# Performance work log

Measured on AMD Instinct MI355X. Metric: run time of the kernel, lower is better.

## Reference

```python
import jax, jax.numpy as jnp
import numpy as np

B, D, T = 16, 512, 2048
H = 2
HD = D // H

def setup_inputs() -> dict:
    key = jax.random.key(0)
    k1, k2, k3, k4 = jax.random.split(key, 4)
    s_in = 1.0 / np.sqrt(D)   # torch default-like uniform init for weight_matrix
    s_t = 1.0 / np.sqrt(T)    # nn.Linear default init bound
    xs = jax.random.normal(k1, (B, D, T), dtype=jnp.float32)
    W_KQ = jax.random.uniform(k2, (D, D), jnp.float32, -s_in, s_in)
    W_PV = jax.random.uniform(k3, (D, D), jnp.float32, -s_in, s_in)
    W_out = jax.random.uniform(k4, (T, T), jnp.float32, -s_t, s_t)
    return {"xs": xs, "W_KQ": W_KQ, "W_PV": W_PV, "W_out": W_out}

def reference(xs, W_KQ, W_PV, W_out):
    b, d, t = xs.shape
    xs_skip = xs[:, :, :-1]                                   # [B, D, T-1]
    # xskq = xs_skip^T @ W_KQ  -> [B, T-1, D]
    xskq = jnp.einsum('bds,dj->bsj', xs_skip, W_KQ)
    # split heads: [B, H, T-1, HD]
    xskq_split = xskq.reshape(b, t - 1, H, HD).transpose(0, 2, 1, 3)
    # xs reshaped to heads along feature dim: [B, H, HD, T]
    xs_r = xs.reshape(b, H, HD, t)
    attn_arg = jnp.matmul(xskq_split, xs_r)                   # [B, H, T-1, T], rho=1
    # NON-STANDARD: softmax over the head axis (size 2)
    sm = jax.nn.softmax(attn_arg, axis=1)
    # W_PV @ xs_skip -> [B, D, T-1], split into heads [B, H, HD, T-1]
    wpvx = jnp.einsum('id,bds->bis', W_PV, xs_skip).reshape(b, H, HD, t - 1)
    f_attn = jnp.matmul(wpvx, sm).reshape(b, d, t)            # [B, D, T]
    # output = Linear(T, T, bias=None) then take last token:
    # out[b, i] = sum_t f_attn[b, i, t] * W_out[T-1, t]
    out = jnp.einsum('bdt,t->bd', f_attn, W_out[-1])
    return out
```

## Files before the change

kernel.cpp:

```cpp
#include <hip/hip_runtime.h>
#include <hip/hip_bf16.h>

#define NB 16
#define ND 512
#define NT 2048
#define TM1 2047
#define NHD 256

typedef __attribute__((ext_vector_type(8))) short bf16x8;
typedef __attribute__((ext_vector_type(4))) float f32x4;
typedef unsigned short ushort_t;
typedef unsigned int uint_t;

#define G0_OFF    0ull
#define G0_ELEMS  (16ull * 2047ull)
#define R0_OFF    32768ull
#define SX_OFF    40960ull
#define ZERO_FLOATS 49152ull
#define WSUM_OFF  49152ull
#define WKQT_OFF  49408ull
#define CHUNK_OFF 180480ull
#define BATCH_US  (2048ull * 512ull)
#define BATCH_FLOATS (2ull * 524288ull)

__device__ __forceinline__ ushort_t f2bf(float x) {
    union { float f; uint_t u; } v; v.f = x;
    uint_t r = v.u + 0x7FFFu + ((v.u >> 16) & 1u);
    return (ushort_t)(r >> 16);
}
__device__ __forceinline__ float bf2f(uint_t u) {
    union { uint_t u; float f; } v; v.u = u << 16;
    return v.f;
}

__device__ __forceinline__ void async_copy16(const ushort_t* g, ushort_t* l) {
    __builtin_amdgcn_global_load_lds(
        (const __attribute__((address_space(1))) void*)g,
        (__attribute__((address_space(3))) void*)l, 16, 0, 0);
}

__global__ __launch_bounds__(256) void k_prep(const float* __restrict__ wkq,
                                              ushort_t* __restrict__ wkqT,
                                              const float* __restrict__ wlast,
                                              float* __restrict__ wsum,
                                              float* __restrict__ zbase) {
    __shared__ float tile[32][33];
    const int j0 = blockIdx.x * 32, d0 = blockIdx.y * 32;
    const int c = threadIdx.x & 31, r = threadIdx.x >> 5;
    #pragma unroll
    for (int i = 0; i < 4; ++i) {
        const int d = r + i * 8;
        tile[d][c] = wkq[(size_t)(d0 + d) * ND + j0 + c];
    }
    __syncthreads();
    #pragma unroll
    for (int i = 0; i < 4; ++i) {
        const int j = r + i * 8;
        wkqT[(size_t)(j0 + j) * ND + d0 + c] = f2bf(tile[c][j]);
    }
    const int bid = blockIdx.y * 16 + blockIdx.x;
    if (threadIdx.x < 192) zbase[bid * 192 + threadIdx.x] = 0.f;
    if (bid == 0) {
        __shared__ float red[256];
        float s = 0.f;
        for (int t = threadIdx.x; t < NT; t += 256) s += wlast[t];
        red[threadIdx.x] = s;
        __syncthreads();
        for (int off = 128; off > 0; off >>= 1) {
            if (threadIdx.x < off) red[threadIdx.x] += red[threadIdx.x + off];
            __syncthreads();
        }
        if (threadIdx.x == 0) *wsum = red[0];
    }
}

__global__ __launch_bounds__(256) void k_cvt_xst(const float* __restrict__ xs,
                                                 ushort_t* __restrict__ xst, int b0) {
    __shared__ float tile[64][257];
    const int t0 = blockIdx.x * 256, d0 = blockIdx.y * 64;
    const int cc = blockIdx.z;
    const float* xb = xs + (size_t)(b0 + cc) * ND * NT;
    ushort_t* xo = xst + (size_t)cc * BATCH_US;
    const int wave = threadIdx.x >> 6, lane = threadIdx.x & 63;
    #pragma unroll
    for (int i = 0; i < 16; ++i) {
        const int row = wave * 16 + i;
        *(float4*)&tile[row][lane * 4] =
            *(const float4*)&xb[(size_t)(d0 + row) * NT + t0 + lane * 4];
    }
    __syncthreads();
    const int c8 = (threadIdx.x & 7) * 8;
    #pragma unroll
    for (int i = 0; i < 8; ++i) {
        const int t = i * 32 + (threadIdx.x >> 3);
        uint_t w[4];
        #pragma unroll
        for (int p = 0; p < 4; ++p)
            w[p] = (uint_t)f2bf(tile[c8 + 2 * p][t]) |
                   ((uint_t)f2bf(tile[c8 + 2 * p + 1][t]) << 16);
        *(uint4*)&xo[(size_t)(t0 + t) * ND + d0 + c8] = *(uint4*)w;
    }
}

__global__ __launch_bounds__(256) void k_qd(const ushort_t* __restrict__ xst,
                                            const ushort_t* __restrict__ wkqT,
                                            ushort_t* __restrict__ qdb) {
    const int j0 = blockIdx.x * 128;
    const int s0 = blockIdx.y * 128;
    const int cc = blockIdx.z;
    __shared__ __align__(16) ushort_t As[128 * 64];
    __shared__ __align__(16) ushort_t Bs[128 * 64];
    const int tid = threadIdx.x;
    const int wave = tid >> 6, lane = tid & 63;
    const int l15 = lane & 15, quad = lane >> 4;
    const int wm = wave >> 1, wn = wave & 1;
    const int swz = l15 & 7;
    const int lrow = lane >> 3;
    const size_t lsrc = (size_t)lrow * ND + (size_t)(((lane & 7) ^ lrow) << 3);
    const ushort_t* xa = xst + (size_t)cc * BATCH_US + (size_t)s0 * ND;
    const ushort_t* wb = wkqT + (size_t)j0 * ND;
    ushort_t* qo = qdb + (size_t)cc * BATCH_US;
    f32x4 acc[4][4];
    #pragma unroll
    for (int mi = 0; mi < 4; ++mi)
        #pragma unroll
        for (int nj = 0; nj < 4; ++nj) acc[mi][nj] = (f32x4){0.f, 0.f, 0.f, 0.f};
    for (int ks = 0; ks < 8; ++ks) {
        const int k0 = ks * 64;
        #pragma unroll
        for (int n = 0; n < 4; ++n) {
            const int rbase = wave * 32 + n * 8;
            async_copy16(xa + (size_t)rbase * ND + k0 + lsrc, &As[rbase * 64]);
            async_copy16(wb + (size_t)rbase * ND + k0 + lsrc, &Bs[rbase * 64]);
        }
        __builtin_amdgcn_s_waitcnt(0);
        __syncthreads();
        #pragma unroll
        for (int kc = 0; kc < 2; ++kc) {
            bf16x8 af[4], bfr[4];
            #pragma unroll
            for (int mi = 0; mi < 4; ++mi)
                af[mi] = *(const bf16x8*)&As[(wm * 64 + mi * 16 + l15) * 64 + (((kc * 4 + quad) ^ swz) << 3)];
            #pragma unroll
            for (int nj = 0; nj < 4; ++nj)
                bfr[nj] = *(const bf16x8*)&Bs[(wn * 64 + nj * 16 + l15) * 64 + (((kc * 4 + quad) ^ swz) << 3)];
            #pragma unroll
            for (int mi = 0; mi < 4; ++mi)
                #pragma unroll
                for (int nj = 0; nj < 4; ++nj)
                    acc[mi][nj] = __builtin_amdgcn_mfma_f32_16x16x32_bf16(af[mi], bfr[nj], acc[mi][nj], 0, 0, 0);
        }
        __syncthreads();
    }
    #pragma unroll
    for (int mi = 0; mi < 4; ++mi) {
        const int srow = s0 + wm * 64 + mi * 16 + quad * 4;
        #pragma unroll
        for (int nj = 0; nj < 4; ++nj) {
            const int jcol = j0 + wn * 64 + nj * 16 + l15;
            const float sgn = (jcol < NHD) ? 1.f : -1.f;
            #pragma unroll
            for (int r = 0; r < 4; ++r)
                qo[(size_t)(srow + r) * ND + jcol] = f2bf(sgn * acc[mi][nj][r]);
        }
    }
}

__global__ __launch_bounds__(256) void k_attn(const ushort_t* __restrict__ qdb,
                                              const ushort_t* __restrict__ xst,
                                              const float* __restrict__ wlast,
                                              float* __restrict__ g0, int b0) {
    const int t0 = blockIdx.x * 128;
    const int s0 = blockIdx.y * 128;
    const int cc = blockIdx.z;
    const int b = b0 + cc;
    __shared__ __align__(16) ushort_t As[128 * 64];
    __shared__ __align__(16) ushort_t Bs[128 * 64];
    const int tid = threadIdx.x;
    const int wave = tid >> 6, lane = tid & 63;
    const int l15 = lane & 15, quad = lane >> 4;
    const int wm = wave >> 1, wn = wave & 1;
    const int swz = l15 & 7;
    const int lrow = lane >> 3;
    const size_t lsrc = (size_t)lrow * ND + (size_t)(((lane & 7) ^ lrow) << 3);
    const ushort_t* qa = qdb + (size_t)cc * BATCH_US + (size_t)s0 * ND;
    const ushort_t* xa = xst + (size_t)cc * BATCH_US + (size_t)t0 * ND;
    f32x4 acc[4][4];
    #pragma unroll
    for (int mi = 0; mi < 4; ++mi)
        #pragma unroll
        for (int nj = 0; nj < 4; ++nj) acc[mi][nj] = (f32x4){0.f, 0.f, 0.f, 0.f};
    for (int ks = 0; ks < 8; ++ks) {
        const int k0 = ks * 64;
        #pragma unroll
        for (int n = 0; n < 4; ++n) {
            const int rbase = wave * 32 + n * 8;
            async_copy16(qa + (size_t)rbase * ND + k0 + lsrc, &As[rbase * 64]);
            async_copy16(xa + (size_t)rbase * ND + k0 + lsrc, &Bs[rbase * 64]);
        }
        __builtin_amdgcn_s_waitcnt(0);
        __syncthreads();
        #pragma unroll
        for (int kc = 0; kc < 2; ++kc) {
            bf16x8 af[4], bfr[4];
            #pragma unroll
            for (int mi = 0; mi < 4; ++mi)
                af[mi] = *(const bf16x8*)&As[(wm * 64 + mi * 16 + l15) * 64 + (((kc * 4 + quad) ^ swz) << 3)];
            #pragma unroll
            for (int nj = 0; nj < 4; ++nj)
                bfr[nj] = *(const bf16x8*)&Bs[(wn * 64 + nj * 16 + l15) * 64 + (((kc * 4 + quad) ^ swz) << 3)];
            #pragma unroll
            for (int mi = 0; mi < 4; ++mi)
                #pragma unroll
                for (int nj = 0; nj < 4; ++nj)
                    acc[mi][nj] = __builtin_amdgcn_mfma_f32_16x16x32_bf16(af[mi], bfr[nj], acc[mi][nj], 0, 0, 0);
        }
        __syncthreads();
    }
    float gp[4][4] = {};
    #pragma unroll
    for (int nj = 0; nj < 4; ++nj) {
        const float wt = wlast[t0 + wn * 64 + nj * 16 + l15];
        #pragma unroll
        for (int mi = 0; mi < 4; ++mi)
            #pragma unroll
            for (int r = 0; r < 4; ++r) {
                const float e = __expf(-acc[mi][nj][r]);
                const float sg = __builtin_amdgcn_rcpf(1.f + e);
                gp[mi][r] = fmaf(sg, wt, gp[mi][r]);
            }
    }
    #pragma unroll
    for (int mi = 0; mi < 4; ++mi)
        #pragma unroll
        for (int r = 0; r < 4; ++r) {
            float v = gp[mi][r];
            v += __shfl_xor(v, 1);
            v += __shfl_xor(v, 2);
            v += __shfl_xor(v, 4);
            v += __shfl_xor(v, 8);
            if (l15 == 0) {
                const int srow = s0 + wm * 64 + mi * 16 + quad * 4 + r;
                if (srow < TM1) atomicAdd(&g0[b * TM1 + srow], v);
            }
        }
}

__global__ __launch_bounds__(256) void k_r(const ushort_t* __restrict__ xst,
                                           const float* __restrict__ g0,
                                           float* __restrict__ r0acc,
                                           float* __restrict__ sxacc, int b0) {
    const int sc = blockIdx.x;
    const int cc = blockIdx.y;
    const int b = b0 + cc;
    const ushort_t* xa = xst + (size_t)cc * BATCH_US;
    const float* g = g0 + b * TM1;
    const int d2 = threadIdx.x;
    float a00 = 0.f, a01 = 0.f, a10 = 0.f, a11 = 0.f;
    const int send = (sc == 31) ? 63 : 64;
    for (int si = 0; si < send; ++si) {
        const int s = sc * 64 + si;
        const float gv = g[s];
        const uint_t pk = *(const uint_t*)&xa[(size_t)s * ND + d2 * 2];
        const float x0 = bf2f(pk & 0xFFFFu);
        const float x1 = bf2f(pk >> 16);
        a00 = fmaf(x0, gv, a00); a01 = fmaf(x1, gv, a01);
        a10 += x0; a11 += x1;
    }
    atomicAdd(&r0acc[b * ND + d2 * 2], a00);
    atomicAdd(&r0acc[b * ND + d2 * 2 + 1], a01);
    atomicAdd(&sxacc[b * ND + d2 * 2], a10);
    atomicAdd(&sxacc[b * ND + d2 * 2 + 1], a11);
}

__global__ __launch_bounds__(256) void k_out(const float* __restrict__ wpv,
                                             const float* __restrict__ r0acc,
                                             const float* __restrict__ sxacc,
                                             const float* __restrict__ wsum,
                                             float* __restrict__ out) {
    const int b = blockIdx.x;
    const int i0 = blockIdx.y * 256;
    __shared__ float rs[1024];
    const float wsv = *wsum;
    for (int i = threadIdx.x; i < ND; i += 256) {
        const float r0 = r0acc[b * ND + i];
        const float sx = sxacc[b * ND + i];
        rs[i] = r0;
        rs[ND + i] = fmaf(wsv, sx, -r0);
    }
    __syncthreads();
    const int i = i0 + threadIdx.x;
    const float* wrow = wpv + (size_t)i * ND;
    const float* rh = rs + (i >> 8) * ND;
    float acc = 0.f;
    for (int dd = 0; dd < ND; dd += 4) {
        const float4 wv = *(const float4*)(wrow + dd);
        acc += wv.x * rh[dd] + wv.y * rh[dd + 1] + wv.z * rh[dd + 2] + wv.w * rh[dd + 3];
    }
    out[b * ND + i] = acc;
}

extern "C" void kernel_launch(void* const* d_in, const int* in_sizes, int n_in,
                              void* d_out, int out_size, void* d_ws, size_t ws_size,
                              hipStream_t stream) {
    (void)in_sizes; (void)n_in; (void)out_size;
    const float* xs   = (const float*)d_in[0];
    const float* wkq  = (const float*)d_in[1];
    const float* wpv  = (const float*)d_in[2];
    const float* wout = (const float*)d_in[3];
    const float* wlast = wout + (size_t)(NT - 1) * NT;

    float* ws    = (float*)d_ws;
    float* g0    = ws + G0_OFF;
    float* r0acc = ws + R0_OFF;
    float* sxacc = ws + SX_OFF;
    float* wsum  = ws + WSUM_OFF;
    ushort_t* wkqT = (ushort_t*)(ws + WKQT_OFF);

    const size_t ws_floats = ws_size / 4;
    size_t avail = (ws_floats > CHUNK_OFF) ? (ws_floats - CHUNK_OFF) : 0;
    int C = (int)(avail / BATCH_FLOATS);
    if (C > NB) C = NB;
    if (C < 1) C = 1;
    ushort_t* qdb = (ushort_t*)(ws + CHUNK_OFF);
    ushort_t* xst = (ushort_t*)(ws + CHUNK_OFF + (size_t)C * 524288ull);

    k_prep<<<dim3(16, 16), 256, 0, stream>>>(wkq, wkqT, wlast, wsum, ws);
    for (int b0 = 0; b0 < NB; b0 += C) {
        const int cb = (NB - b0 < C) ? (NB - b0) : C;
        k_cvt_xst<<<dim3(8, 8, cb), 256, 0, stream>>>(xs, xst, b0);
        k_qd     <<<dim3(4, 16, cb),  256, 0, stream>>>(xst, wkqT, qdb);
        k_attn   <<<dim3(16, 16, cb), 256, 0, stream>>>(qdb, xst, wlast, g0, b0);
        k_r      <<<dim3(32, cb),     256, 0, stream>>>(xst, g0, r0acc, sxacc, b0);
    }
    k_out<<<dim3(NB, 2), 256, 0, stream>>>(wpv, r0acc, sxacc, wsum, (float*)d_out);
}
```

Baseline: 291.9 us.

## Rewrite attention GEMM as 256x256 double-buffered ping-pong tile with LDS reduction

The k_attn kernel moves from 128x128 tiles with 4 waves and a single LDS buffer to 256x256 tiles with 8 waves. It double-buffers A and B in LDS, issuing async global-to-LDS loads interleaved with MFMA phases, waiting with vmcnt and raising wave priority around MFMA bursts. The per-row sigmoid-weighted sums are first reduced in LDS and then written with one global atomic per row instead of one per wave fragment. This targets memory stalls and atomic traffic, at the cost of higher register and LDS pressure and many barriers per k-step.

```diff
diff --git a/kernel.cpp b/kernel.cpp
--- a/kernel.cpp
+++ b/kernel.cpp
@@ -38,6 +38,11 @@
         (const __attribute__((address_space(1))) void*)g,
         (__attribute__((address_space(3))) void*)l, 16, 0, 0);
 }
+
+#define FENCE() asm volatile("" ::: "memory")
+#define BARRIER() do { FENCE(); __builtin_amdgcn_s_barrier(); FENCE(); } while (0)
+#define WAITVM4() asm volatile("s_waitcnt vmcnt(4)" ::: "memory")
+#define WAITVM0() asm volatile("s_waitcnt vmcnt(0)" ::: "memory")
 
 __global__ __launch_bounds__(256) void k_prep(const float* __restrict__ wkq,
                                               ushort_t* __restrict__ wkqT,
@@ -166,84 +171,153 @@
     }
 }
 
-__global__ __launch_bounds__(256) void k_attn(const ushort_t* __restrict__ qdb,
-                                              const ushort_t* __restrict__ xst,
-                                              const float* __restrict__ wlast,
-                                              float* __restrict__ g0, int b0) {
-    const int t0 = blockIdx.x * 128;
-    const int s0 = blockIdx.y * 128;
+__device__ __forceinline__ void ld_frag4(bf16x8 (&dst)[4][2], const ushort_t* buf,
+                                         int rbase, int l15, int quad, int swz) {
+    #pragma unroll
+    for (int i = 0; i < 4; ++i)
+        #pragma unroll
+        for (int kc = 0; kc < 2; ++kc)
+            dst[i][kc] = *(const bf16x8*)&buf[(rbase + i * 16 + l15) * 64 + (((kc * 4 + quad) ^ swz) << 3)];
+}
+__device__ __forceinline__ void ld_frag2(bf16x8 (&dst)[2][2], const ushort_t* buf,
+                                         int rbase, int l15, int quad, int swz) {
+    #pragma unroll
+    for (int i = 0; i < 2; ++i)
+        #pragma unroll
+        for (int kc = 0; kc < 2; ++kc)
+            dst[i][kc] = *(const bf16x8*)&buf[(rbase + i * 16 + l15) * 64 + (((kc * 4 + quad) ^ swz) << 3)];
+}
+__device__ __forceinline__ void mfma8(f32x4 (&acc)[8][4], const bf16x8 (&a)[4][2],
+                                      const bf16x8 (&bb)[2][2], int mbase, int nbase) {
+    __builtin_amdgcn_s_setprio(1);
+    #pragma unroll
+    for (int kc = 0; kc < 2; ++kc)
+        #pragma unroll
+        for (int mi = 0; mi < 4; ++mi)
+            #pragma unroll
+            for (int nj = 0; nj < 2; ++nj)
+                acc[mbase + mi][nbase + nj] = __builtin_amdgcn_mfma_f32_16x16x32_bf16(
+                    a[mi][kc], bb[nj][kc], acc[mbase + mi][nbase + nj], 0, 0, 0);
+    __builtin_amdgcn_s_setprio(0);
+}
+
+__global__ __launch_bounds__(512, 2) void k_attn(const ushort_t* __restrict__ qdb,
+                                                 const ushort_t* __restrict__ xst,
+                                                 const float* __restrict__ wlast,
+                                                 float* __restrict__ g0, int b0) {
+    const int t0 = blockIdx.x * 256;
+    const int s0 = blockIdx.y * 256;
     const int cc = blockIdx.z;
     const int b = b0 + cc;
-    __shared__ __align__(16) ushort_t As[128 * 64];
-    __shared__ __align__(16) ushort_t Bs[128 * 64];
+    __shared__ __align__(16) ushort_t smA[2][16384];
+    __shared__ __align__(16) ushort_t smB[2][16384];
+    __shared__ float lds_g[256];
     const int tid = threadIdx.x;
     const int wave = tid >> 6, lane = tid & 63;
     const int l15 = lane & 15, quad = lane >> 4;
-    const int wm = wave >> 1, wn = wave & 1;
+    const int wm = wave >> 2, wn = wave & 3;
     const int swz = l15 & 7;
     const int lrow = lane >> 3;
     const size_t lsrc = (size_t)lrow * ND + (size_t)(((lane & 7) ^ lrow) << 3);
-    const ushort_t* qa = qdb + (size_t)cc * BATCH_US + (size_t)s0 * ND;
-    const ushort_t* xa = xst + (size_t)cc * BATCH_US + (size_t)t0 * ND;
-    f32x4 acc[4][4];
-    #pragma unroll
-    for (int mi = 0; mi < 4; ++mi)
+    const ushort_t* Ag = qdb + (size_t)cc * BATCH_US + (size_t)s0 * ND;
+    const ushort_t* Bg = xst + (size_t)cc * BATCH_US + (size_t)t0 * ND;
+
+#define STAGE(gb_, buf_, kt_, h_) do {                                        \
+        const ushort_t* g_ = (gb_) + (size_t)((h_) * 128 + wave * 8) * ND +   \
+                             (kt_) * 64 + lsrc;                               \
+        ushort_t* l_ = (buf_) + (h_) * 8192 + wave * 512;                     \
+        async_copy16(g_, l_);                                                 \
+        async_copy16(g_ + (size_t)64 * ND, l_ + 4096);                        \
+    } while (0)
+
+    f32x4 acc[8][4];
+    #pragma unroll
+    for (int mi = 0; mi < 8; ++mi)
         #pragma unroll
         for (int nj = 0; nj < 4; ++nj) acc[mi][nj] = (f32x4){0.f, 0.f, 0.f, 0.f};
-    for (int ks = 0; ks < 8; ++ks) {
-        const int k0 = ks * 64;
-        #pragma unroll
-        for (int n = 0; n < 4; ++n) {
-            const int rbase = wave * 32 + n * 8;
-            async_copy16(qa + (size_t)rbase * ND + k0 + lsrc, &As[rbase * 64]);
-            async_copy16(xa + (size_t)rbase * ND + k0 + lsrc, &Bs[rbase * 64]);
-        }
-        __builtin_amdgcn_s_waitcnt(0);
-        __syncthreads();
-        #pragma unroll
-        for (int kc = 0; kc < 2; ++kc) {
-            bf16x8 af[4], bfr[4];
-            #pragma unroll
-            for (int mi = 0; mi < 4; ++mi)
-                af[mi] = *(const bf16x8*)&As[(wm * 64 + mi * 16 + l15) * 64 + (((kc * 4 + quad) ^ swz) << 3)];
-            #pragma unroll
-            for (int nj = 0; nj < 4; ++nj)
-                bfr[nj] = *(const bf16x8*)&Bs[(wn * 64 + nj * 16 + l15) * 64 + (((kc * 4 + quad) ^ swz) << 3)];
-            #pragma unroll
-            for (int mi = 0; mi < 4; ++mi)
-                #pragma unroll
-                for (int nj = 0; nj < 4; ++nj)
-                    acc[mi][nj] = __builtin_amdgcn_mfma_f32_16x16x32_bf16(af[mi], bfr[nj], acc[mi][nj], 0, 0, 0);
-        }
-        __syncthreads();
-    }
-    float gp[4][4] = {};
-    #pragma unroll
-    for (int nj = 0; nj < 4; ++nj) {
-        const float wt = wlast[t0 + wn * 64 + nj * 16 + l15];
-        #pragma unroll
-        for (int mi = 0; mi < 4; ++mi)
-            #pragma unroll
-            for (int r = 0; r < 4; ++r) {
+    bf16x8 a[4][2], br[2][2][2];
+
+    STAGE(Bg, smB[0], 0, 0); STAGE(Bg, smB[0], 0, 1);
+    STAGE(Ag, smA[0], 0, 0); STAGE(Ag, smA[0], 0, 1);
+    STAGE(Bg, smB[1], 1, 0); STAGE(Bg, smB[1], 1, 1);
+    WAITVM4();
+    BARRIER();
+
+    #pragma unroll
+    for (int j = 0; j < 4; ++j) {
+        const int kO = 2 * j + 1;
+        ld_frag4(a, smA[0], wm * 128, l15, quad, swz);
+        ld_frag2(br[0], smB[0], wn * 64, l15, quad, swz);
+        STAGE(Ag, smA[1], kO, 0);
+        BARRIER();
+        mfma8(acc, a, br[0], 0, 0);
+        BARRIER();
+        ld_frag2(br[1], smB[0], wn * 64 + 32, l15, quad, swz);
+        STAGE(Ag, smA[1], kO, 1);
+        BARRIER();
+        mfma8(acc, a, br[1], 0, 2);
+        BARRIER();
+        ld_frag4(a, smA[0], wm * 128 + 64, l15, quad, swz);
+        if (j < 3) STAGE(Bg, smB[0], 2 * j + 2, 0);
+        BARRIER();
+        mfma8(acc, a, br[0], 4, 0);
+        BARRIER();
+        if (j < 3) STAGE(Bg, smB[0], 2 * j + 2, 1);
+        BARRIER();
+        mfma8(acc, a, br[1], 4, 2);
+        if (j < 3) { WAITVM4(); } else { WAITVM0(); }
+        BARRIER();
+        ld_frag4(a, smA[1], wm * 128, l15, quad, swz);
+        ld_frag2(br[0], smB[1], wn * 64, l15, quad, swz);
+        if (j < 3) STAGE(Ag, smA[0], 2 * j + 2, 0);
+        BARRIER();
+        mfma8(acc, a, br[0], 0, 0);
+        BARRIER();
+        ld_frag2(br[1], smB[1], wn * 64 + 32, l15, quad, swz);
+        if (j < 3) STAGE(Ag, smA[0], 2 * j + 2, 1);
+        BARRIER();
+        mfma8(acc, a, br[1], 0, 2);
+        BARRIER();
+        ld_frag4(a, smA[1], wm * 128 + 64, l15, quad, swz);
+        if (j < 3) STAGE(Bg, smB[1], kO + 2, 0);
+        BARRIER();
+        mfma8(acc, a, br[0], 4, 0);
+        BARRIER();
+        if (j < 3) STAGE(Bg, smB[1], kO + 2, 1);
+        BARRIER();
+        mfma8(acc, a, br[1], 4, 2);
+        if (j < 3) WAITVM4();
+        BARRIER();
+    }
+#undef STAGE
+
+    if (tid < 256) lds_g[tid] = 0.f;
+    __syncthreads();
+    float wt[4];
+    #pragma unroll
+    for (int nj = 0; nj < 4; ++nj) wt[nj] = wlast[t0 + wn * 64 + nj * 16 + l15];
+    #pragma unroll
+    for (int mi = 0; mi < 8; ++mi) {
+        #pragma unroll
+        for (int r = 0; r < 4; ++r) {
+            float v = 0.f;
+            #pragma unroll
+            for (int nj = 0; nj < 4; ++nj) {
                 const float e = __expf(-acc[mi][nj][r]);
-                const float sg = __builtin_amdgcn_rcpf(1.f + e);
-                gp[mi][r] = fmaf(sg, wt, gp[mi][r]);
+                v = fmaf(__builtin_amdgcn_rcpf(1.f + e), wt[nj], v);
             }
-    }
-    #pragma unroll
-    for (int mi = 0; mi < 4; ++mi)
-        #pragma unroll
-        for (int r = 0; r < 4; ++r) {
-            float v = gp[mi][r];
             v += __shfl_xor(v, 1);
             v += __shfl_xor(v, 2);
             v += __shfl_xor(v, 4);
             v += __shfl_xor(v, 8);
-            if (l15 == 0) {
-                const int srow = s0 + wm * 64 + mi * 16 + quad * 4 + r;
-                if (srow < TM1) atomicAdd(&g0[b * TM1 + srow], v);
-            }
+            if (l15 == 0) atomicAdd(&lds_g[wm * 128 + mi * 16 + quad * 4 + r], v);
         }
+    }
+    __syncthreads();
+    if (tid < 256) {
+        const int srow = s0 + tid;
+        if (srow < TM1) atomicAdd(&g0[b * TM1 + srow], lds_g[tid]);
+    }
 }
 
 __global__ __launch_bounds__(256) void k_r(const ushort_t* __restrict__ xst,
@@ -330,7 +404,7 @@
         const int cb = (NB - b0 < C) ? (NB - b0) : C;
         k_cvt_xst<<<dim3(8, 8, cb), 256, 0, stream>>>(xs, xst, b0);
         k_qd     <<<dim3(4, 16, cb),  256, 0, stream>>>(xst, wkqT, qdb);
-        k_attn   <<<dim3(16, 16, cb), 256, 0, stream>>>(qdb, xst, wlast, g0, b0);
+        k_attn   <<<dim3(8, 8, cb),  512, 0, stream>>>(qdb, xst, wlast, g0, b0);
         k_r      <<<dim3(32, cb),     256, 0, stream>>>(xst, g0, r0acc, sxacc, b0);
     }
     k_out<<<dim3(NB, 2), 256, 0, stream>>>(wpv, r0acc, sxacc, wsum, (float*)d_out);
```

Result: faster. 275.0 us (-5.8%).

## Fuse Q projection and attention-score GEMM into one LDS-resident kernel

Applied to the files above, without the earlier changes.

Merges the weight-prep kernel into the xs conversion kernel, run by the blocks of the first batch chunk. Replaces the separate k_qd and k_attn kernels with one 512-thread kernel per 128-row strip. The kernel computes the signed Q tile into a 128KB LDS panel, then streams x^T rows from global memory into registers with double buffering. It reduces the sigmoid-weighted scores into LDS before one plain store to g0. This removes the qdb global round trip, a launch, and the global atomics. In exchange there is one large block per CU with far fewer blocks, and B operands are read straight from global memory without LDS sharing.

```diff
diff --git a/kernel.cpp b/kernel.cpp
--- a/kernel.cpp
+++ b/kernel.cpp
@@ -13,15 +13,13 @@
 typedef unsigned int uint_t;
 
 #define G0_OFF    0ull
-#define G0_ELEMS  (16ull * 2047ull)
 #define R0_OFF    32768ull
 #define SX_OFF    40960ull
-#define ZERO_FLOATS 49152ull
 #define WSUM_OFF  49152ull
 #define WKQT_OFF  49408ull
 #define CHUNK_OFF 180480ull
 #define BATCH_US  (2048ull * 512ull)
-#define BATCH_FLOATS (2ull * 524288ull)
+#define BATCH_FLOATS 524288ull
 
 __device__ __forceinline__ ushort_t f2bf(float x) {
     union { float f; uint_t u; } v; v.f = x;
@@ -39,43 +37,17 @@
         (__attribute__((address_space(3))) void*)l, 16, 0, 0);
 }
 
-__global__ __launch_bounds__(256) void k_prep(const float* __restrict__ wkq,
-                                              ushort_t* __restrict__ wkqT,
-                                              const float* __restrict__ wlast,
-                                              float* __restrict__ wsum,
-                                              float* __restrict__ zbase) {
-    __shared__ float tile[32][33];
-    const int j0 = blockIdx.x * 32, d0 = blockIdx.y * 32;
-    const int c = threadIdx.x & 31, r = threadIdx.x >> 5;
-    #pragma unroll
-    for (int i = 0; i < 4; ++i) {
-        const int d = r + i * 8;
-        tile[d][c] = wkq[(size_t)(d0 + d) * ND + j0 + c];
-    }
-    __syncthreads();
-    #pragma unroll
-    for (int i = 0; i < 4; ++i) {
-        const int j = r + i * 8;
-        wkqT[(size_t)(j0 + j) * ND + d0 + c] = f2bf(tile[c][j]);
-    }
-    const int bid = blockIdx.y * 16 + blockIdx.x;
-    if (threadIdx.x < 192) zbase[bid * 192 + threadIdx.x] = 0.f;
-    if (bid == 0) {
-        __shared__ float red[256];
-        float s = 0.f;
-        for (int t = threadIdx.x; t < NT; t += 256) s += wlast[t];
-        red[threadIdx.x] = s;
-        __syncthreads();
-        for (int off = 128; off > 0; off >>= 1) {
-            if (threadIdx.x < off) red[threadIdx.x] += red[threadIdx.x + off];
-            __syncthreads();
-        }
-        if (threadIdx.x == 0) *wsum = red[0];
-    }
-}
+#define FENCE() asm volatile("" ::: "memory")
+#define BARRIER() do { FENCE(); __builtin_amdgcn_s_barrier(); FENCE(); } while (0)
+#define WAITVM0() asm volatile("s_waitcnt vmcnt(0)" ::: "memory")
 
 __global__ __launch_bounds__(256) void k_cvt_xst(const float* __restrict__ xs,
-                                                 ushort_t* __restrict__ xst, int b0) {
+                                                 ushort_t* __restrict__ xst, int b0,
+                                                 const float* __restrict__ wkq,
+                                                 ushort_t* __restrict__ wkqT,
+                                                 const float* __restrict__ wlast,
+                                                 float* __restrict__ wsum,
+                                                 float* __restrict__ zbase) {
     __shared__ float tile[64][257];
     const int t0 = blockIdx.x * 256, d0 = blockIdx.y * 64;
     const int cc = blockIdx.z;
@@ -100,150 +72,202 @@
                    ((uint_t)f2bf(tile[c8 + 2 * p + 1][t]) << 16);
         *(uint4*)&xo[(size_t)(t0 + t) * ND + d0 + c8] = *(uint4*)w;
     }
-}
-
-__global__ __launch_bounds__(256) void k_qd(const ushort_t* __restrict__ xst,
-                                            const ushort_t* __restrict__ wkqT,
-                                            ushort_t* __restrict__ qdb) {
-    const int j0 = blockIdx.x * 128;
-    const int s0 = blockIdx.y * 128;
-    const int cc = blockIdx.z;
-    __shared__ __align__(16) ushort_t As[128 * 64];
-    __shared__ __align__(16) ushort_t Bs[128 * 64];
+    if (cc == 0 && b0 == 0) {
+        __shared__ float ptile[32][33];
+        const int bid = blockIdx.y * 8 + blockIdx.x;
+        const int c = threadIdx.x & 31, r = threadIdx.x >> 5;
+        #pragma unroll 1
+        for (int q = 0; q < 4; ++q) {
+            const int job = bid * 4 + q;
+            const int j0 = (job & 15) * 32, dd0 = (job >> 4) * 32;
+            __syncthreads();
+            #pragma unroll
+            for (int i = 0; i < 4; ++i)
+                ptile[r + i * 8][c] = wkq[(size_t)(dd0 + r + i * 8) * ND + j0 + c];
+            __syncthreads();
+            #pragma unroll
+            for (int i = 0; i < 4; ++i)
+                wkqT[(size_t)(j0 + r + i * 8) * ND + dd0 + c] = f2bf(ptile[c][r + i * 8]);
+        }
+        #pragma unroll
+        for (int k = 0; k < 3; ++k)
+            zbase[bid * 768 + k * 256 + threadIdx.x] = 0.f;
+        if (bid == 0) {
+            __shared__ float red[256];
+            float s = 0.f;
+            for (int t = threadIdx.x; t < NT; t += 256) s += wlast[t];
+            red[threadIdx.x] = s;
+            __syncthreads();
+            for (int off = 128; off > 0; off >>= 1) {
+                if (threadIdx.x < off) red[threadIdx.x] += red[threadIdx.x + off];
+                __syncthreads();
+            }
+            if (threadIdx.x == 0) *wsum = red[0];
+        }
+    }
+}
+
+__global__ __launch_bounds__(512, 2) void k_fused(const ushort_t* __restrict__ xst,
+                                                  const ushort_t* __restrict__ wkqT,
+                                                  const float* __restrict__ wlast,
+                                                  float* __restrict__ g0, int b0) {
+    __shared__ __align__(16) ushort_t panel[8][8192];
+    __shared__ float lds_g[128];
+    const int lin = blockIdx.x + gridDim.x * blockIdx.y;
+    const int nwg8 = (gridDim.x * gridDim.y) >> 3;
+    const int logical = (lin & 7) * nwg8 + (lin >> 3);
+    const int st = logical & 15;
+    const int cc = logical >> 4;
+    const int s0 = st * 128;
+    const int b = b0 + cc;
+
     const int tid = threadIdx.x;
     const int wave = tid >> 6, lane = tid & 63;
     const int l15 = lane & 15, quad = lane >> 4;
-    const int wm = wave >> 1, wn = wave & 1;
-    const int swz = l15 & 7;
+    const ushort_t* xb = xst + (size_t)cc * BATCH_US;
+
     const int lrow = lane >> 3;
     const size_t lsrc = (size_t)lrow * ND + (size_t)(((lane & 7) ^ lrow) << 3);
-    const ushort_t* xa = xst + (size_t)cc * BATCH_US + (size_t)s0 * ND;
-    const ushort_t* wb = wkqT + (size_t)j0 * ND;
-    ushort_t* qo = qdb + (size_t)cc * BATCH_US;
+    {
+        const ushort_t* Ag = xb + (size_t)s0 * ND;
+        #pragma unroll
+        for (int kt = 0; kt < 8; ++kt) {
+            const ushort_t* gp = Ag + (size_t)(wave * 16) * ND + kt * 64 + lsrc;
+            async_copy16(gp, &panel[kt][wave * 1024]);
+            async_copy16(gp + (size_t)8 * ND, &panel[kt][wave * 1024 + 512]);
+        }
+    }
+    if (tid < 128) lds_g[tid] = 0.f;
+    WAITVM0();
+    BARRIER();
+
+    {
+        f32x4 a1[8][4];
+        #pragma unroll
+        for (int mi = 0; mi < 8; ++mi)
+            #pragma unroll
+            for (int nj = 0; nj < 4; ++nj) a1[mi][nj] = (f32x4){0.f, 0.f, 0.f, 0.f};
+        const ushort_t* Wg = wkqT + (size_t)(wave * 64) * ND;
+        #pragma unroll 1
+        for (int kt = 0; kt < 8; ++kt) {
+            bf16x8 bw[4][2];
+            #pragma unroll
+            for (int nj = 0; nj < 4; ++nj)
+                #pragma unroll
+                for (int kc = 0; kc < 2; ++kc)
+                    bw[nj][kc] = *(const bf16x8*)&Wg[(size_t)(nj * 16 + l15) * ND +
+                                                     kt * 64 + ((kc * 4 + quad) << 3)];
+            __builtin_amdgcn_s_setprio(1);
+            #pragma unroll
+            for (int mi = 0; mi < 8; ++mi) {
+                const int row = mi * 16 + l15;
+                const bf16x8 af0 = *(const bf16x8*)&panel[kt][row * 64 + ((quad ^ (row & 7)) << 3)];
+                const bf16x8 af1 = *(const bf16x8*)&panel[kt][row * 64 + (((4 + quad) ^ (row & 7)) << 3)];
+                #pragma unroll
+                for (int nj = 0; nj < 4; ++nj) {
+                    a1[mi][nj] = __builtin_amdgcn_mfma_f32_16x16x32_bf16(af0, bw[nj][0], a1[mi][nj], 0, 0, 0);
+                    a1[mi][nj] = __builtin_amdgcn_mfma_f32_16x16x32_bf16(af1, bw[nj][1], a1[mi][nj], 0, 0, 0);
+                }
+            }
+            __builtin_amdgcn_s_setprio(0);
+        }
+        BARRIER();
+        const float sgn = (wave < 4) ? 1.f : -1.f;
+        #pragma unroll
+        for (int mi = 0; mi < 8; ++mi)
+            #pragma unroll
+            for (int nj = 0; nj < 4; ++nj)
+                #pragma unroll
+                for (int r = 0; r < 4; ++r) {
+                    const int srow = mi * 16 + quad * 4 + r;
+                    const int c = nj * 16 + l15;
+                    panel[wave][srow * 64 + ((((c >> 3) ^ (srow & 7)) << 3) | (c & 7))] =
+                        f2bf(sgn * a1[mi][nj][r]);
+                }
+    }
+    BARRIER();
+
+    const int wm = wave >> 2, wn = wave & 3;
     f32x4 acc[4][4];
     #pragma unroll
     for (int mi = 0; mi < 4; ++mi)
         #pragma unroll
         for (int nj = 0; nj < 4; ++nj) acc[mi][nj] = (f32x4){0.f, 0.f, 0.f, 0.f};
-    for (int ks = 0; ks < 8; ++ks) {
-        const int k0 = ks * 64;
-        #pragma unroll
-        for (int n = 0; n < 4; ++n) {
-            const int rbase = wave * 32 + n * 8;
-            async_copy16(xa + (size_t)rbase * ND + k0 + lsrc, &As[rbase * 64]);
-            async_copy16(wb + (size_t)rbase * ND + k0 + lsrc, &Bs[rbase * 64]);
-        }
-        __builtin_amdgcn_s_waitcnt(0);
-        __syncthreads();
-        #pragma unroll
-        for (int kc = 0; kc < 2; ++kc) {
-            bf16x8 af[4], bfr[4];
-            #pragma unroll
-            for (int mi = 0; mi < 4; ++mi)
-                af[mi] = *(const bf16x8*)&As[(wm * 64 + mi * 16 + l15) * 64 + (((kc * 4 + quad) ^ swz) << 3)];
-            #pragma unroll
-            for (int nj = 0; nj < 4; ++nj)
-                bfr[nj] = *(const bf16x8*)&Bs[(wn * 64 + nj * 16 + l15) * 64 + (((kc * 4 + quad) ^ swz) << 3)];
-            #pragma unroll
-            for (int mi = 0; mi < 4; ++mi)
-                #pragma unroll
-                for (int nj = 0; nj < 4; ++nj)
-                    acc[mi][nj] = __builtin_amdgcn_mfma_f32_16x16x32_bf16(af[mi], bfr[nj], acc[mi][nj], 0, 0, 0);
-        }
-        __syncthreads();
-    }
-    #pragma unroll
-    for (int mi = 0; mi < 4; ++mi) {
-        const int srow = s0 + wm * 64 + mi * 16 + quad * 4;
-        #pragma unroll
-        for (int nj = 0; nj < 4; ++nj) {
-            const int jcol = j0 + wn * 64 + nj * 16 + l15;
-            const float sgn = (jcol < NHD) ? 1.f : -1.f;
-            #pragma unroll
-            for (int r = 0; r < 4; ++r)
-                qo[(size_t)(srow + r) * ND + jcol] = f2bf(sgn * acc[mi][nj][r]);
-        }
-    }
-}
-
-__global__ __launch_bounds__(256) void k_attn(const ushort_t* __restrict__ qdb,
-                                              const ushort_t* __restrict__ xst,
-                                              const float* __restrict__ wlast,
-                                              float* __restrict__ g0, int b0) {
-    const int t0 = blockIdx.x * 128;
-    const int s0 = blockIdx.y * 128;
-    const int cc = blockIdx.z;
-    const int b = b0 + cc;
-    __shared__ __align__(16) ushort_t As[128 * 64];
-    __shared__ __align__(16) ushort_t Bs[128 * 64];
-    const int tid = threadIdx.x;
-    const int wave = tid >> 6, lane = tid & 63;
-    const int l15 = lane & 15, quad = lane >> 4;
-    const int wm = wave >> 1, wn = wave & 1;
-    const int swz = l15 & 7;
-    const int lrow = lane >> 3;
-    const size_t lsrc = (size_t)lrow * ND + (size_t)(((lane & 7) ^ lrow) << 3);
-    const ushort_t* qa = qdb + (size_t)cc * BATCH_US + (size_t)s0 * ND;
-    const ushort_t* xa = xst + (size_t)cc * BATCH_US + (size_t)t0 * ND;
-    f32x4 acc[4][4];
-    #pragma unroll
-    for (int mi = 0; mi < 4; ++mi)
-        #pragma unroll
-        for (int nj = 0; nj < 4; ++nj) acc[mi][nj] = (f32x4){0.f, 0.f, 0.f, 0.f};
-    for (int ks = 0; ks < 8; ++ks) {
-        const int k0 = ks * 64;
-        #pragma unroll
-        for (int n = 0; n < 4; ++n) {
-            const int rbase = wave * 32 + n * 8;
-            async_copy16(qa + (size_t)rbase * ND + k0 + lsrc, &As[rbase * 64]);
-            async_copy16(xa + (size_t)rbase * ND + k0 + lsrc, &Bs[rbase * 64]);
-        }
-        __builtin_amdgcn_s_waitcnt(0);
-        __syncthreads();
-        #pragma unroll
-        for (int kc = 0; kc < 2; ++kc) {
-            bf16x8 af[4], bfr[4];
-            #pragma unroll
-            for (int mi = 0; mi < 4; ++mi)
-                af[mi] = *(const bf16x8*)&As[(wm * 64 + mi * 16 + l15) * 64 + (((kc * 4 + quad) ^ swz) << 3)];
-            #pragma unroll
-            for (int nj = 0; nj < 4; ++nj)
-                bfr[nj] = *(const bf16x8*)&Bs[(wn * 64 + nj * 16 + l15) * 64 + (((kc * 4 + quad) ^ swz) << 3)];
-            #pragma unroll
-            for (int mi = 0; mi < 4; ++mi)
-                #pragma unroll
-                for (int nj = 0; nj < 4; ++nj)
-                    acc[mi][nj] = __builtin_amdgcn_mfma_f32_16x16x32_bf16(af[mi], bfr[nj], acc[mi][nj], 0, 0, 0);
-        }
-        __syncthreads();
-    }
-    float gp[4][4] = {};
-    #pragma unroll
-    for (int nj = 0; nj < 4; ++nj) {
-        const float wt = wlast[t0 + wn * 64 + nj * 16 + l15];
-        #pragma unroll
-        for (int mi = 0; mi < 4; ++mi)
-            #pragma unroll
-            for (int r = 0; r < 4; ++r) {
-                const float e = __expf(-acc[mi][nj][r]);
-                const float sg = __builtin_amdgcn_rcpf(1.f + e);
-                gp[mi][r] = fmaf(sg, wt, gp[mi][r]);
-            }
-    }
-    #pragma unroll
-    for (int mi = 0; mi < 4; ++mi)
-        #pragma unroll
-        for (int r = 0; r < 4; ++r) {
-            float v = gp[mi][r];
-            v += __shfl_xor(v, 1);
-            v += __shfl_xor(v, 2);
-            v += __shfl_xor(v, 4);
-            v += __shfl_xor(v, 8);
-            if (l15 == 0) {
-                const int srow = s0 + wm * 64 + mi * 16 + quad * 4 + r;
-                if (srow < TM1) atomicAdd(&g0[b * TM1 + srow], v);
-            }
-        }
+    bf16x8 bx0[4][2], bx1[4][2];
+
+#define LOADB(dst_, s_) do {                                                  \
+        const int kt_ = (s_) & 7, tt_ = (s_) >> 3;                            \
+        const ushort_t* bb_ = xb + (size_t)(tt_ * 256 + wn * 64) * ND + kt_ * 64; \
+        _Pragma("unroll")                                                     \
+        for (int nj = 0; nj < 4; ++nj)                                        \
+            _Pragma("unroll")                                                 \
+            for (int kc = 0; kc < 2; ++kc)                                    \
+                dst_[nj][kc] = *(const bf16x8*)&bb_[(size_t)(nj * 16 + l15) * ND + \
+                                                    ((kc * 4 + quad) << 3)];  \
+    } while (0)
+#define PV(bx_, s_) do {                                                      \
+        const int kt_ = (s_) & 7;                                             \
+        __builtin_amdgcn_s_setprio(1);                                        \
+        _Pragma("unroll")                                                     \
+        for (int mi = 0; mi < 4; ++mi) {                                      \
+            const int row_ = wm * 64 + mi * 16 + l15;                         \
+            const bf16x8 af0_ = *(const bf16x8*)&panel[kt_][row_ * 64 + ((quad ^ (row_ & 7)) << 3)]; \
+            const bf16x8 af1_ = *(const bf16x8*)&panel[kt_][row_ * 64 + (((4 + quad) ^ (row_ & 7)) << 3)]; \
+            _Pragma("unroll")                                                 \
+            for (int nj = 0; nj < 4; ++nj) {                                  \
+                acc[mi][nj] = __builtin_amdgcn_mfma_f32_16x16x32_bf16(af0_, bx_[nj][0], acc[mi][nj], 0, 0, 0); \
+                acc[mi][nj] = __builtin_amdgcn_mfma_f32_16x16x32_bf16(af1_, bx_[nj][1], acc[mi][nj], 0, 0, 0); \
+            }                                                                 \
+        }                                                                     \
+        __builtin_amdgcn_s_setprio(0);                                        \
+    } while (0)
+#define DUMP(tt_) do {                                                        \
+        float wt_[4];                                                         \
+        _Pragma("unroll")                                                     \
+        for (int nj = 0; nj < 4; ++nj)                                        \
+            wt_[nj] = wlast[(tt_) * 256 + wn * 64 + nj * 16 + l15];           \
+        _Pragma("unroll")                                                     \
+        for (int mi = 0; mi < 4; ++mi)                                        \
+            _Pragma("unroll")                                                 \
+            for (int r = 0; r < 4; ++r) {                                     \
+                float v_ = 0.f;                                               \
+                _Pragma("unroll")                                             \
+                for (int nj = 0; nj < 4; ++nj) {                              \
+                    const float e_ = __expf(-acc[mi][nj][r]);                 \
+                    v_ = fmaf(__builtin_amdgcn_rcpf(1.f + e_), wt_[nj], v_);  \
+                }                                                             \
+                v_ += __shfl_xor(v_, 1);                                      \
+                v_ += __shfl_xor(v_, 2);                                      \
+                v_ += __shfl_xor(v_, 4);                                      \
+                v_ += __shfl_xor(v_, 8);                                      \
+                if (l15 == 0)                                                 \
+                    atomicAdd(&lds_g[wm * 64 + mi * 16 + quad * 4 + r], v_);  \
+            }                                                                 \
+        _Pragma("unroll")                                                     \
+        for (int mi = 0; mi < 4; ++mi)                                        \
+            _Pragma("unroll")                                                 \
+            for (int nj = 0; nj < 4; ++nj) acc[mi][nj] = (f32x4){0.f, 0.f, 0.f, 0.f}; \
+    } while (0)
+
+    LOADB(bx0, 0);
+    #pragma unroll 1
+    for (int jp = 0; jp < 32; ++jp) {
+        const int sA = 2 * jp, sB = 2 * jp + 1;
+        LOADB(bx1, sB);
+        PV(bx0, sA);
+        if (jp < 31) LOADB(bx0, sB + 1);
+        PV(bx1, sB);
+        if ((sB & 7) == 7) DUMP(sB >> 3);
+    }
+#undef LOADB
+#undef PV
+#undef DUMP
+
+    __syncthreads();
+    if (tid < 128) {
+        const int srow = s0 + tid;
+        if (srow < TM1) g0[b * TM1 + srow] = lds_g[tid];
+    }
 }
 
 __global__ __launch_bounds__(256) void k_r(const ushort_t* __restrict__ xst,
@@ -322,16 +346,15 @@
     int C = (int)(avail / BATCH_FLOATS);
     if (C > NB) C = NB;
     if (C < 1) C = 1;
-    ushort_t* qdb = (ushort_t*)(ws + CHUNK_OFF);
-    ushort_t* xst = (ushort_t*)(ws + CHUNK_OFF + (size_t)C * 524288ull);
-
-    k_prep<<<dim3(16, 16), 256, 0, stream>>>(wkq, wkqT, wlast, wsum, ws);
+    if (C > 1 && (C & 1)) C -= 1;
+    ushort_t* xst = (ushort_t*)(ws + CHUNK_OFF);
+
     for (int b0 = 0; b0 < NB; b0 += C) {
         const int cb = (NB - b0 < C) ? (NB - b0) : C;
-        k_cvt_xst<<<dim3(8, 8, cb), 256, 0, stream>>>(xs, xst, b0);
-        k_qd     <<<dim3(4, 16, cb),  256, 0, stream>>>(xst, wkqT, qdb);
-        k_attn   <<<dim3(16, 16, cb), 256, 0, stream>>>(qdb, xst, wlast, g0, b0);
-        k_r      <<<dim3(32, cb),     256, 0, stream>>>(xst, g0, r0acc, sxacc, b0);
+        k_cvt_xst<<<dim3(8, 8, cb), 256, 0, stream>>>(xs, xst, b0,
+                                                      wkq, wkqT, wlast, wsum, ws);
+        k_fused  <<<dim3(16, cb),  512, 0, stream>>>(xst, wkqT, wlast, g0, b0);
+        k_r      <<<dim3(32, cb),  256, 0, stream>>>(xst, g0, r0acc, sxacc, b0);
     }
     k_out<<<dim3(NB, 2), 256, 0, stream>>>(wpv, r0acc, sxacc, wsum, (float*)d_out);
 }
```

After: 290.6 us. No clear change (-0.4%).
